# Optimization experiments

Hardware: AMD Instinct MI355X
Metric: run time of the kernel (lower is better)

The kernel has to match this reference:

```python
import jax, jax.numpy as jnp
import numpy as np

N_NODES = 50000
N_EDGES = 1600000
IN_DIM = 256
HID = 128
BATCH = 16384
EDGE_FEAT = 6
BN_EPS = 1e-5


def _glorot(key, shape):
    fan_in, fan_out = shape[0], shape[1]
    lim = float(np.sqrt(6.0 / (fan_in + fan_out)))
    return jax.random.uniform(key, shape, jnp.float32, -lim, lim)


def setup_inputs() -> dict:
    key = jax.random.key(0)
    ks = jax.random.split(key, 20)
    return {
        "x": jax.random.normal(ks[0], (N_NODES, IN_DIM), jnp.float32),
        "edge_index": jax.random.randint(ks[1], (2, N_EDGES), 0, N_NODES, jnp.int64 if jax.config.jax_enable_x64 else jnp.int32),
        "src_nodes": jax.random.randint(ks[2], (BATCH,), 0, N_NODES),
        "tgt_nodes": jax.random.randint(ks[3], (BATCH,), 0, N_NODES),
        "edge_features": jax.random.uniform(ks[4], (BATCH, EDGE_FEAT), jnp.float32),
        # SAGEConv layer 0: lin_l (aggregated neighbors, has bias), lin_r (root, no bias)
        "sage_wl0": _glorot(ks[5], (IN_DIM, HID)),
        "sage_b0": jnp.zeros((HID,), jnp.float32),
        "sage_wr0": _glorot(ks[6], (IN_DIM, HID)),
        # SAGEConv layer 1
        "sage_wl1": _glorot(ks[7], (HID, HID)),
        "sage_b1": jnp.zeros((HID,), jnp.float32),
        "sage_wr1": _glorot(ks[8], (HID, HID)),
        # edge_processor: Linear(6, 64)
        "ep_w": _glorot(ks[9], (EDGE_FEAT, HID // 2)),
        "ep_b": jnp.zeros((HID // 2,), jnp.float32),
        # predictor: Linear(320,128) -> ReLU -> BN(128) -> Linear(128,64) -> ReLU -> Linear(64,1) -> Sigmoid
        "p1_w": _glorot(ks[10], (2 * HID + HID // 2, HID)),
        "p1_b": jnp.zeros((HID,), jnp.float32),
        "bn_gamma": jnp.ones((HID,), jnp.float32),
        "bn_beta": jnp.zeros((HID,), jnp.float32),
        "bn_mean": jnp.zeros((HID,), jnp.float32),
        "bn_var": jnp.ones((HID,), jnp.float32),
        "p2_w": _glorot(ks[11], (HID, HID // 2)),
        "p2_b": jnp.zeros((HID // 2,), jnp.float32),
        "p3_w": _glorot(ks[12], (HID // 2, 1)),
        "p3_b": jnp.zeros((1,), jnp.float32),
    }


def _sage_conv(h, src, dst, w_l, b, w_r):
    # PyG SAGEConv(mean): out_i = W_l @ mean_{j in N(i)} h_j + b + W_r @ h_i
    n = h.shape[0]
    agg = jax.ops.segment_sum(h[src], dst, num_segments=n)  # [N, d]
    deg = jax.ops.segment_sum(jnp.ones((src.shape[0],), h.dtype), dst, num_segments=n)
    mean = agg / jnp.maximum(deg, 1.0)[:, None]
    return mean @ w_l + b + h @ w_r


def reference(x, edge_index, src_nodes, tgt_nodes, edge_features,
              sage_wl0, sage_b0, sage_wr0, sage_wl1, sage_b1, sage_wr1,
              ep_w, ep_b, p1_w, p1_b, bn_gamma, bn_beta, bn_mean, bn_var,
              p2_w, p2_b, p3_w, p3_b):
    src, dst = edge_index[0], edge_index[1]
    h = _sage_conv(x, src, dst, sage_wl0, sage_b0, sage_wr0)
    h = jax.nn.relu(h)  # dropout is identity in eval mode
    h = _sage_conv(h, src, dst, sage_wl1, sage_b1, sage_wr1)
    src_emb = h[src_nodes]  # [B, HID]
    tgt_emb = h[tgt_nodes]  # [B, HID]
    edge_proc = jax.nn.relu(edge_features @ ep_w + ep_b)  # [B, HID//2]
    combined = jnp.concatenate([src_emb, tgt_emb, edge_proc], axis=1)  # [B, 320]
    z = jax.nn.relu(combined @ p1_w + p1_b)
    z = (z - bn_mean) / jnp.sqrt(bn_var + BN_EPS) * bn_gamma + bn_beta  # BN eval mode
    z = jax.nn.relu(z @ p2_w + p2_b)
    return jax.nn.sigmoid(z @ p3_w + p3_b)  # [B, 1]
```

## Files before the change

### kernel.cpp

```cpp
#include <hip/hip_runtime.h>
#include <hip/hip_bf16.h>

#define N_NODES 50000
#define N_EDGES 1600000
#define BATCH   16384
#define HID     128
#define NBUCK   782
#define NBLK    256
#define EPB     6250

using short8  = __attribute__((ext_vector_type(8))) short;
using floatx4 = __attribute__((ext_vector_type(4))) float;
using floatv4 = __attribute__((ext_vector_type(4))) float;
using float2v = __attribute__((ext_vector_type(2))) float;
using uint2v  = __attribute__((ext_vector_type(2))) unsigned;
using uintx4  = __attribute__((ext_vector_type(4))) unsigned;
typedef unsigned short ushort_t;

__device__ __forceinline__ float bflo(unsigned u){ return __uint_as_float(u << 16); }
__device__ __forceinline__ float bfhi(unsigned u){ return __uint_as_float(u & 0xffff0000u); }
__device__ __forceinline__ float bf1(ushort_t u){ return __uint_as_float(((unsigned)u) << 16); }
__device__ __forceinline__ ushort_t f2bf(float f){
    unsigned u = __float_as_uint(f);
    return (ushort_t)((u + 0x7fffu + ((u >> 16) & 1u)) >> 16);
}
__device__ __forceinline__ int geti(const void* p, long long i, int is64){
    return is64 ? (int)((const long long*)p)[i] : ((const int*)p)[i];
}
__device__ __forceinline__ float2v up2(unsigned u){
    float2v r; r.x = bflo(u); r.y = bfhi(u); return r;
}

__global__ void k_detect(const unsigned* __restrict__ xbits,
                         const unsigned* __restrict__ eibits, int* flags){
    __shared__ int f[2];
    int t = threadIdx.x;
    if (t < 2) f[t] = 0;
    __syncthreads();
    unsigned u = xbits[t];
    unsigned e0 = (u >> 7)  & 0xFF;
    unsigned e1 = (u >> 23) & 0xFF;
    if (e0 >= 140 || e1 >= 140) atomicOr(&f[0], 1);
    if (eibits[2*t + 1] != 0)   atomicOr(&f[1], 1);
    __syncthreads();
    if (t == 0){ flags[0] = f[0]; flags[1] = f[1] ? 0 : 1; }
}

#define NT 19
struct ConvDesc { const void* src[NT]; int cum[NT + 1]; };
__global__ void k_conv(ConvDesc d, ushort_t* __restrict__ dst, const int* __restrict__ flags){
    int i = blockIdx.x*256 + threadIdx.x;
    if (i >= d.cum[NT]) return;
    int seg = 0;
    while (i >= d.cum[seg + 1]) seg++;
    int off = i - d.cum[seg];
    ushort_t v;
    if (flags[0]) v = f2bf(((const float*)d.src[seg])[off]);
    else          v = ((const ushort_t*)d.src[seg])[off];
    dst[i] = v;
}

#define OFF_WL0 0
#define OFF_WR0 32768
#define OFF_WL1 65536
#define OFF_WR1 81920
#define OFF_B0  98304
#define OFF_B1  98432
#define OFF_EPW 98560
#define OFF_EPB 98944
#define OFF_P1W 99008
#define OFF_P1B 139968
#define OFF_BNG 140096
#define OFF_BNB 140224
#define OFF_BNM 140352
#define OFF_BNV 140480
#define OFF_P2W 140608
#define OFF_P2B 148800
#define OFF_P3W 148864
#define OFF_EF  148928
#define OFF_P3B 247232
#define CW_TOT  247233

#define PACK_TOT 147584
__global__ void k_pack(const ushort_t* __restrict__ cw,
                       ushort_t* __restrict__ bp0, ushort_t* __restrict__ bp1,
                       ushort_t* __restrict__ bpp1, ushort_t* __restrict__ bpp2,
                       float* __restrict__ bnf){
    int i = blockIdx.x*256 + threadIdx.x;
    if (i < 65536){
        int j = i & 7, lane = (i >> 3) & 63, c = (i >> 9) & 15, kk = i >> 13;
        int k = kk*32 + (lane >> 4)*8 + j;
        int n = c*16 + (lane & 15);
        bp0[i] = (n < 128) ? cw[OFF_WL0 + k*128 + n] : cw[OFF_WR0 + k*128 + (n-128)];
    } else if (i < 98304){
        int i2 = i - 65536;
        int j = i2 & 7, lane = (i2 >> 3) & 63, c = (i2 >> 9) & 15, kk = i2 >> 13;
        int k = kk*32 + (lane >> 4)*8 + j;
        int n = c*16 + (lane & 15);
        bp1[i2] = (n < 128) ? cw[OFF_WL1 + k*128 + n] : cw[OFF_WR1 + k*128 + (n-128)];
    } else if (i < 139264){
        int i2 = i - 98304;
        int j = i2 & 7, lane = (i2 >> 3) & 63, ct = (i2 >> 9) & 7, kk = i2 >> 12;
        int k = kk*32 + (lane >> 4)*8 + j;
        int n = ct*16 + (lane & 15);
        bpp1[i2] = cw[OFF_P1W + k*128 + n];
    } else if (i < 147456){
        int i2 = i - 139264;
        int j = i2 & 7, lane = (i2 >> 3) & 63, ct = (i2 >> 9) & 3, kk = i2 >> 11;
        int k = kk*32 + (lane >> 4)*8 + j;
        int n = ct*16 + (lane & 15);
        bpp2[i2] = cw[OFF_P2W + k*64 + n];
    } else if (i < PACK_TOT){
        int n = i - 147456;
        float g = bf1(cw[OFF_BNG + n]), b = bf1(cw[OFF_BNB + n]);
        float m = bf1(cw[OFF_BNM + n]), v = bf1(cw[OFF_BNV + n]);
        float sc = g / sqrtf(v + 1e-5f);
        bnf[n] = sc; bnf[128 + n] = b - m*sc;
    }
}

__global__ __launch_bounds__(256)
void kb_hist(const void* __restrict__ ei, int* __restrict__ hist,
             const int* __restrict__ flags){
    __shared__ int lh[NBUCK];
    for (int i = threadIdx.x; i < NBUCK; i += 256) lh[i] = 0;
    __syncthreads();
    int i64 = flags[1];
    int e0 = blockIdx.x * EPB;
    for (int e = e0 + threadIdx.x; e < e0 + EPB; e += 256){
        int d = geti(ei, (long long)N_EDGES + e, i64);
        atomicAdd(&lh[d >> 6], 1);
    }
    __syncthreads();
    for (int i = threadIdx.x; i < NBUCK; i += 256)
        hist[i * NBLK + blockIdx.x] = lh[i];
}

__global__ __launch_bounds__(256)
void kb_scancol(int* __restrict__ hist, int* __restrict__ btot){
    __shared__ int sh[256];
    int b = blockIdx.x, t = threadIdx.x;
    int v = hist[b*NBLK + t];
    sh[t] = v; __syncthreads();
    for (int o = 1; o < 256; o <<= 1){
        int x = (t >= o) ? sh[t-o] : 0;
        __syncthreads();
        sh[t] += x;
        __syncthreads();
    }
    hist[b*NBLK + t] = sh[t] - v;
    if (t == 255) btot[b] = sh[255];
}

__global__ __launch_bounds__(1024)
void kb_scanbase(const int* __restrict__ btot, int* __restrict__ bbase,
                 int* __restrict__ off){
    __shared__ int sh[1024];
    int t = threadIdx.x;
    int v = (t < NBUCK) ? btot[t] : 0;
    sh[t] = v; __syncthreads();
    for (int o = 1; o < 1024; o <<= 1){
        int x = (t >= o) ? sh[t-o] : 0;
        __syncthreads();
        sh[t] += x;
        __syncthreads();
    }
    if (t < NBUCK) bbase[t] = sh[t] - v;
    if (t == 0){ bbase[NBUCK] = N_EDGES; off[N_NODES] = N_EDGES; }
}

__global__ __launch_bounds__(256)
void kb_scatter(const void* __restrict__ ei, const int* __restrict__ hist,
                const int* __restrict__ bbase, unsigned* __restrict__ ebuf,
                const int* __restrict__ flags){
    __shared__ int lcur[NBUCK];
    for (int i = threadIdx.x; i < NBUCK; i += 256)
        lcur[i] = bbase[i] + hist[i*NBLK + blockIdx.x];
    __syncthreads();
    int i64 = flags[1];
    int e0 = blockIdx.x * EPB;
    for (int e = e0 + threadIdx.x; e < e0 + EPB; e += 256){
        int s = geti(ei, e, i64);
        int d = geti(ei, (long long)N_EDGES + e, i64);
        int p = atomicAdd(&lcur[d >> 6], 1);
        ebuf[p] = (unsigned)s | ((unsigned)(d & 63) << 16);
    }
}

__global__ __launch_bounds__(256)
void kb_csr(const unsigned* __restrict__ ebuf, const int* __restrict__ bbase,
            ushort_t* __restrict__ csr, int* __restrict__ off){
    __shared__ int ldeg[64];
    int b = blockIdx.x, t = threadIdx.x;
    int ebase = bbase[b], eend = bbase[b+1];
    if (t < 64) ldeg[t] = 0;
    __syncthreads();
    for (int i = ebase + t; i < eend; i += 256)
        atomicAdd(&ldeg[(ebuf[i] >> 16) & 63], 1);
    __syncthreads();
    if (t < 64){
        int v = ldeg[t];
        int sum = v;
        #pragma unroll
        for (int o = 1; o < 64; o <<= 1){
            int x = __shfl_up(sum, o, 64);
            if (t >= o) sum += x;
        }
        int excl = sum - v;
        int node = b*64 + t;
        if (node < N_NODES) off[node] = ebase + excl;
        ldeg[t] = excl;
    }
    __syncthreads();
    for (int i = ebase + t; i < eend; i += 256){
        unsigned u = ebuf[i];
        int p = atomicAdd(&ldeg[(u >> 16) & 63], 1);
        csr[ebase + p] = (ushort_t)(u & 0xffffu);
    }
}

template<int KSTEPS, bool CHECKBF>
__global__ __launch_bounds__(256)
void k_gemm2(const ushort_t* __restrict__ A, const ushort_t* __restrict__ Bp,
             ushort_t* __restrict__ out, int M, const int* __restrict__ flags)
{
    if (CHECKBF && flags[0]) return;
    const int lane = threadIdx.x & 63;
    const int w    = threadIdx.x >> 6;
    const int rg   = w >> 1;
    const int cg   = w & 1;
    const int l16  = lane & 15;
    const int q    = lane >> 4;
    const int S    = KSTEPS * 32;
    const int m_base = blockIdx.x * 32 + rg * 16;

    int m = m_base + l16;
    bool ok = (m < M);
    const ushort_t* arow = A + (size_t)(ok ? m : 0) * S + q*8;
    const short8* bbase = (const short8*)Bp + lane;

    floatx4 acc[8] = {};
    for (int kk = 0; kk < KSTEPS; ++kk){
        short8 a = {0,0,0,0,0,0,0,0};
        if (ok) a = *(const short8*)(arow + kk*32);
        #pragma unroll
        for (int ci = 0; ci < 8; ++ci){
            short8 b = bbase[(kk*16 + cg*8 + ci)*64];
            acc[ci] = __builtin_amdgcn_mfma_f32_16x16x32_bf16(a, b, acc[ci], 0, 0, 0);
        }
    }

    int row_b = m_base + q*4;
    #pragma unroll
    for (int r = 0; r < 4; ++r){
        int row = row_b + r;
        if (row < M){
            #pragma unroll
            for (int ci = 0; ci < 8; ++ci)
                out[(size_t)row*256 + cg*128 + ci*16 + l16] = f2bf(acc[ci][r]);
        }
    }
}

__global__ __launch_bounds__(256)
void k_gemm2f(const float* __restrict__ Af, const ushort_t* __restrict__ Bp,
              ushort_t* __restrict__ out, int M, const int* __restrict__ flags)
{
    if (!flags[0]) return;
    const int KSTEPS = 8;
    const int lane = threadIdx.x & 63;
    const int w    = threadIdx.x >> 6;
    const int rg   = w >> 1;
    const int cg   = w & 1;
    const int l16  = lane & 15;
    const int q    = lane >> 4;
    const int S    = KSTEPS * 32;
    const int m_base = blockIdx.x * 32 + rg * 16;

    int m = m_base + l16;
    bool ok = (m < M);
    const float* arow = Af + (size_t)(ok ? m : 0) * S + q*8;
    const short8* bbase = (const short8*)Bp + lane;

    floatx4 acc[8] = {};
    for (int kk = 0; kk < KSTEPS; ++kk){
        union { unsigned u[4]; short8 s; } cv;
        cv.u[0]=0; cv.u[1]=0; cv.u[2]=0; cv.u[3]=0;
        if (ok){
            floatv4 f0 = *(const floatv4*)(arow + kk*32);
            floatv4 f1 = *(const floatv4*)(arow + kk*32 + 4);
            cv.u[0] = __builtin_amdgcn_perm(__float_as_uint(f0.y), __float_as_uint(f0.x), 0x07060302);
            cv.u[1] = __builtin_amdgcn_perm(__float_as_uint(f0.w), __float_as_uint(f0.z), 0x07060302);
            cv.u[2] = __builtin_amdgcn_perm(__float_as_uint(f1.y), __float_as_uint(f1.x), 0x07060302);
            cv.u[3] = __builtin_amdgcn_perm(__float_as_uint(f1.w), __float_as_uint(f1.z), 0x07060302);
        }
        #pragma unroll
        for (int ci = 0; ci < 8; ++ci){
            short8 b = bbase[(kk*16 + cg*8 + ci)*64];
            acc[ci] = __builtin_amdgcn_mfma_f32_16x16x32_bf16(cv.s, b, acc[ci], 0, 0, 0);
        }
    }

    int row_b = m_base + q*4;
    #pragma unroll
    for (int r = 0; r < 4; ++r){
        int row = row_b + r;
        if (row < M){
            #pragma unroll
            for (int ci = 0; ci < 8; ++ci)
                out[(size_t)row*256 + cg*128 + ci*16 + l16] = f2bf(acc[ci][r]);
        }
    }
}

__global__ __launch_bounds__(256)
void k_agg(const int* __restrict__ off, const ushort_t* __restrict__ csr,
           const ushort_t* __restrict__ yr, const ushort_t* __restrict__ bias,
           ushort_t* __restrict__ out, int do_relu)
{
    int v = blockIdx.x*4 + (threadIdx.x >> 6);
    if (v >= N_NODES) return;
    const int l = threadIdx.x & 63;
    const int g = l >> 4;
    const int c = l & 15;
    int e0 = off[v], e1 = off[v+1];
    const ushort_t* yb = yr + c*8;

    float2v A0[4] = {}, A1[4] = {}, A2[4] = {}, A3[4] = {};
    int p = e0;
    for (; p + 16 <= e1; p += 16){
        int u0 = csr[p + g];
        int u1 = csr[p + 4 + g];
        int u2 = csr[p + 8 + g];
        int u3 = csr[p + 12 + g];
        uintx4 d0 = *(const uintx4*)(yb + (size_t)u0*256);
        uintx4 d1 = *(const uintx4*)(yb + (size_t)u1*256);
        uintx4 d2 = *(const uintx4*)(yb + (size_t)u2*256);
        uintx4 d3 = *(const uintx4*)(yb + (size_t)u3*256);
        A0[0] += up2(d0.x); A0[1] += up2(d0.y); A0[2] += up2(d0.z); A0[3] += up2(d0.w);
        A1[0] += up2(d1.x); A1[1] += up2(d1.y); A1[2] += up2(d1.z); A1[3] += up2(d1.w);
        A2[0] += up2(d2.x); A2[1] += up2(d2.y); A2[2] += up2(d2.z); A2[3] += up2(d2.w);
        A3[0] += up2(d3.x); A3[1] += up2(d3.y); A3[2] += up2(d3.z); A3[3] += up2(d3.w);
    }
    for (; p + 4 <= e1; p += 4){
        int u0 = csr[p + g];
        uintx4 d0 = *(const uintx4*)(yb + (size_t)u0*256);
        A0[0] += up2(d0.x); A0[1] += up2(d0.y); A0[2] += up2(d0.z); A0[3] += up2(d0.w);
    }
    if (p + g < e1){
        int u1 = csr[p + g];
        uintx4 d1 = *(const uintx4*)(yb + (size_t)u1*256);
        A1[0] += up2(d1.x); A1[1] += up2(d1.y); A1[2] += up2(d1.z); A1[3] += up2(d1.w);
    }
    #pragma unroll
    for (int j = 0; j < 4; ++j) A0[j] += A1[j] + A2[j] + A3[j];

    float a0=A0[0].x, a1=A0[0].y, a2=A0[1].x, a3=A0[1].y;
    float a4=A0[2].x, a5=A0[2].y, a6=A0[3].x, a7=A0[3].y;
    #pragma unroll
    for (int m = 16; m <= 32; m <<= 1){
        a0 += __shfl_xor(a0, m, 64); a1 += __shfl_xor(a1, m, 64);
        a2 += __shfl_xor(a2, m, 64); a3 += __shfl_xor(a3, m, 64);
        a4 += __shfl_xor(a4, m, 64); a5 += __shfl_xor(a5, m, 64);
        a6 += __shfl_xor(a6, m, 64); a7 += __shfl_xor(a7, m, 64);
    }
    if (g == 0){
        float inv = 1.f / (float)max(e1 - e0, 1);
        uintx4 rr = *(const uintx4*)(yr + (size_t)v*256 + 128 + c*8);
        uintx4 bb = *(const uintx4*)(bias + c*8);
        float v0 = a0*inv + bflo(rr.x) + bflo(bb.x);
        float v1 = a1*inv + bfhi(rr.x) + bfhi(bb.x);
        float v2 = a2*inv + bflo(rr.y) + bflo(bb.y);
        float v3 = a3*inv + bfhi(rr.y) + bfhi(bb.y);
        float v4 = a4*inv + bflo(rr.z) + bflo(bb.z);
        float v5 = a5*inv + bfhi(rr.z) + bfhi(bb.z);
        float v6 = a6*inv + bflo(rr.w) + bflo(bb.w);
        float v7 = a7*inv + bfhi(rr.w) + bfhi(bb.w);
        if (do_relu){
            v0=fmaxf(v0,0.f); v1=fmaxf(v1,0.f); v2=fmaxf(v2,0.f); v3=fmaxf(v3,0.f);
            v4=fmaxf(v4,0.f); v5=fmaxf(v5,0.f); v6=fmaxf(v6,0.f); v7=fmaxf(v7,0.f);
        }
        uintx4 o;
        o.x = (unsigned)f2bf(v0) | ((unsigned)f2bf(v1) << 16);
        o.y = (unsigned)f2bf(v2) | ((unsigned)f2bf(v3) << 16);
        o.z = (unsigned)f2bf(v4) | ((unsigned)f2bf(v5) << 16);
        o.w = (unsigned)f2bf(v6) | ((unsigned)f2bf(v7) << 16);
        *(uintx4*)(out + (size_t)v*128 + c*8) = o;
    }
}

__global__ __launch_bounds__(256)
void k_pred2(const ushort_t* __restrict__ h2,
             const void* __restrict__ srcn, const void* __restrict__ tgtn,
             const ushort_t* __restrict__ cw, const ushort_t* __restrict__ bpp1,
             const ushort_t* __restrict__ bpp2, const float* __restrict__ bnf,
             void* __restrict__ outp, const int* __restrict__ flags)
{
    __shared__ ushort_t comb[64][328];
    __shared__ ushort_t zbuf[64][136];
    __shared__ ushort_t z2buf[64][68];
    __shared__ float    partial[4][64];
    __shared__ int      sid[64], tid_[64];

    const int t    = threadIdx.x;
    const int lane = t & 63;
    const int w    = t >> 6;
    const int l16  = lane & 15;
    const int q    = lane >> 4;
    const int row0 = blockIdx.x * 64;
    const int i64  = flags[1];

    if (t < 64){ sid[t] = geti(srcn, row0 + t, i64); tid_[t] = geti(tgtn, row0 + t, i64); }
    __syncthreads();

    const unsigned* h2u = (const unsigned*)h2;
    #pragma unroll 4
    for (int r = w*16; r < w*16 + 16; ++r){
        unsigned us = h2u[(size_t)sid[r]*64 + lane];
        unsigned ut = h2u[(size_t)tid_[r]*64 + lane];
        *(unsigned*)&comb[r][2*lane]       = us;
        *(unsigned*)&comb[r][128 + 2*lane] = ut;
    }
    {
        int r = t >> 2, c0 = (t & 3) * 16;
        float efv[6];
        #pragma unroll
        for (int k = 0; k < 6; ++k) efv[k] = bf1(cw[OFF_EF + (row0 + r)*6 + k]);
        #pragma unroll
        for (int c = 0; c < 16; ++c){
            int n = c0 + c;
            float a = bf1(cw[OFF_EPB + n]);
            #pragma unroll
            for (int k = 0; k < 6; ++k) a += efv[k] * bf1(cw[OFF_EPW + k*64 + n]);
            comb[r][256 + n] = f2bf(fmaxf(a, 0.f));
        }
    }
    __syncthreads();

    floatx4 acc[4][2] = {};
    for (int kk = 0; kk < 10; ++kk){
        short8 a[4];
        #pragma unroll
        for (int rt = 0; rt < 4; ++rt)
            a[rt] = *(const short8*)&comb[rt*16 + l16][kk*32 + q*8];
        #pragma unroll
        for (int ci = 0; ci < 2; ++ci){
            short8 b = *(const short8*)&bpp1[(((kk*8) + (w*2 + ci))*64 + lane)*8];
            #pragma unroll
            for (int rt = 0; rt < 4; ++rt)
                acc[rt][ci] = __builtin_amdgcn_mfma_f32_16x16x32_bf16(a[rt], b, acc[rt][ci], 0, 0, 0);
        }
    }
    #pragma unroll
    for (int ci = 0; ci < 2; ++ci){
        int n = w*32 + ci*16 + l16;
        float b1v = bf1(cw[OFF_P1B + n]);
        float sc = bnf[n], sh = bnf[128 + n];
        #pragma unroll
        for (int rt = 0; rt < 4; ++rt)
            #pragma unroll
            for (int r = 0; r < 4; ++r){
                float v = fmaxf(acc[rt][ci][r] + b1v, 0.f) * sc + sh;
                zbuf[rt*16 + q*4 + r][n] = f2bf(v);
            }
    }
    __syncthreads();

    floatx4 acc2[4] = {};
    for (int kk = 0; kk < 4; ++kk){
        short8 b = *(const short8*)&bpp2[(((kk*4) + w)*64 + lane)*8];
        #pragma unroll
        for (int rt = 0; rt < 4; ++rt){
            short8 a = *(const short8*)&zbuf[rt*16 + l16][kk*32 + q*8];
            acc2[rt] = __builtin_amdgcn_mfma_f32_16x16x32_bf16(a, b, acc2[rt], 0, 0, 0);
        }
    }
    {
        int n = w*16 + l16;
        float b2v = bf1(cw[OFF_P2B + n]);
        #pragma unroll
        for (int rt = 0; rt < 4; ++rt)
            #pragma unroll
            for (int r = 0; r < 4; ++r)
                z2buf[rt*16 + q*4 + r][n] = f2bf(fmaxf(acc2[rt][r] + b2v, 0.f));
    }
    __syncthreads();

    {
        int r = t & 63, seg = t >> 6;
        float s = 0.f;
        #pragma unroll
        for (int c = 0; c < 16; ++c){
            int n = seg*16 + c;
            s += bf1(z2buf[r][n]) * bf1(cw[OFF_P3W + n]);
        }
        partial[seg][r] = s;
    }
    __syncthreads();
    if (t < 64){
        float zf = partial[0][t] + partial[1][t] + partial[2][t] + partial[3][t] + bf1(cw[OFF_P3B]);
        float sg = 1.f / (1.f + __expf(-zf));
        if (flags[0]) ((float*)outp)[row0 + t] = sg;
        else          ((ushort_t*)outp)[row0 + t] = f2bf(sg);
    }
}

extern "C" void kernel_launch(void* const* d_in, const int* in_sizes, int n_in,
                              void* d_out, int out_size, void* d_ws, size_t ws_size,
                              hipStream_t stream)
{
    const void* x    = d_in[0];
    const void* ei   = d_in[1];
    const void* srcn = d_in[2];
    const void* tgtn = d_in[3];

    char* p = (char*)d_ws;
    auto carve = [&](size_t bytes)->char*{ char* r = p; p += (bytes + 511) & ~size_t(511); return r; };
    int* flags = (int*)carve(64);
    int* off   = (int*)carve((N_NODES+1)*4);
    int* btot  = (int*)carve(NBUCK*4);
    int* bbase = (int*)carve((NBUCK+1)*4);
    ushort_t* csr = (ushort_t*)carve((size_t)N_EDGES*2);
    ushort_t* yr  = (ushort_t*)carve((size_t)N_NODES*256*2);
    ushort_t* h   = (ushort_t*)carve((size_t)N_NODES*128*2);
    ushort_t* cw  = (ushort_t*)carve((size_t)CW_TOT*2);
    ushort_t* bp0 = (ushort_t*)carve((size_t)65536*2);
    ushort_t* bp1 = (ushort_t*)carve((size_t)32768*2);
    ushort_t* bpp1= (ushort_t*)carve((size_t)40960*2);
    ushort_t* bpp2= (ushort_t*)carve((size_t)8192*2);
    float*    bnf = (float*)carve(256*4);

    int*      hist = (int*)yr;
    unsigned* ebuf = (unsigned*)((char*)yr + 8u*1024*1024);

    k_detect<<<1, 256, 0, stream>>>((const unsigned*)x, (const unsigned*)ei, flags);

    ConvDesc cd;
    const int srcidx[NT] = {5,7,8,10,6,9,11,12,13,14,15,16,17,18,19,20,21,4,22};
    const int lens[NT]   = {32768,32768,16384,16384,128,128,384,64,40960,128,128,128,128,128,8192,64,64,98304,1};
    int run = 0;
    for (int i = 0; i < NT; ++i){ cd.src[i] = d_in[srcidx[i]]; cd.cum[i] = run; run += lens[i]; }
    cd.cum[NT] = run;
    k_conv<<<(CW_TOT+255)/256, 256, 0, stream>>>(cd, cw, flags);
    k_pack<<<(PACK_TOT+255)/256, 256, 0, stream>>>(cw, bp0, bp1, bpp1, bpp2, bnf);

    kb_hist    <<<NBLK, 256, 0, stream>>>(ei, hist, flags);
    kb_scancol <<<NBUCK, 256, 0, stream>>>(hist, btot);
    kb_scanbase<<<1, 1024, 0, stream>>>(btot, bbase, off);
    kb_scatter <<<NBLK, 256, 0, stream>>>(ei, hist, bbase, ebuf, flags);
    kb_csr     <<<NBUCK, 256, 0, stream>>>(ebuf, bbase, csr, off);

    int gblocks = (N_NODES + 31) / 32;
    k_gemm2<8, true><<<gblocks, 256, 0, stream>>>((const ushort_t*)x, bp0, yr, N_NODES, flags);
    k_gemm2f<<<gblocks, 256, 0, stream>>>((const float*)x, bp0, yr, N_NODES, flags);
    k_agg<<<(N_NODES+3)/4, 256, 0, stream>>>(off, csr, yr, cw+OFF_B0, h, 1);
    k_gemm2<4, false><<<gblocks, 256, 0, stream>>>(h, bp1, yr, N_NODES, flags);
    k_agg<<<(N_NODES+3)/4, 256, 0, stream>>>(off, csr, yr, cw+OFF_B1, h, 0);

    k_pred2<<<BATCH/64, 256, 0, stream>>>(h, srcn, tgtn, cw, bpp1, bpp2, bnf, d_out, flags);
}
```

Baseline: 342.2 us.

## Fuse independent preprocessing stages into shared launches to overlap GEMM with CSR build

Independent kernels are merged into combined launches where a block-index split picks the work: weight conversion runs alongside the edge histogram, weight packing alongside the column scan, and the layer-0 GEMM is split in halves that share launches with the edge scatter and CSR build. To allow this, the hist/ebuf scratch moves from the yr buffer, which the GEMM now writes concurrently, into the h buffer. The aim is fewer launches and idle gaps, with compute-heavy GEMM blocks filling the GPU while the atomic-bound sort kernels run. The cost is more branchy kernels whose LDS use and register pressure are set by the largest branch.

```diff
diff --git a/kernel.cpp b/kernel.cpp
--- a/kernel.cpp
+++ b/kernel.cpp
@@ -9,6 +9,11 @@
 #define NBLK    256
 #define EPB     6250
 
+#define CONVB   967
+#define PACKB   577
+#define G0A     782
+#define G0B     781
+
 using short8  = __attribute__((ext_vector_type(8))) short;
 using floatx4 = __attribute__((ext_vector_type(4))) float;
 using floatv4 = __attribute__((ext_vector_type(4))) float;
@@ -29,35 +34,6 @@
 }
 __device__ __forceinline__ float2v up2(unsigned u){
     float2v r; r.x = bflo(u); r.y = bfhi(u); return r;
-}
-
-__global__ void k_detect(const unsigned* __restrict__ xbits,
-                         const unsigned* __restrict__ eibits, int* flags){
-    __shared__ int f[2];
-    int t = threadIdx.x;
-    if (t < 2) f[t] = 0;
-    __syncthreads();
-    unsigned u = xbits[t];
-    unsigned e0 = (u >> 7)  & 0xFF;
-    unsigned e1 = (u >> 23) & 0xFF;
-    if (e0 >= 140 || e1 >= 140) atomicOr(&f[0], 1);
-    if (eibits[2*t + 1] != 0)   atomicOr(&f[1], 1);
-    __syncthreads();
-    if (t == 0){ flags[0] = f[0]; flags[1] = f[1] ? 0 : 1; }
-}
-
-#define NT 19
-struct ConvDesc { const void* src[NT]; int cum[NT + 1]; };
-__global__ void k_conv(ConvDesc d, ushort_t* __restrict__ dst, const int* __restrict__ flags){
-    int i = blockIdx.x*256 + threadIdx.x;
-    if (i >= d.cum[NT]) return;
-    int seg = 0;
-    while (i >= d.cum[seg + 1]) seg++;
-    int off = i - d.cum[seg];
-    ushort_t v;
-    if (flags[0]) v = f2bf(((const float*)d.src[seg])[off]);
-    else          v = ((const ushort_t*)d.src[seg])[off];
-    dst[i] = v;
 }
 
 #define OFF_WL0 0
@@ -80,76 +56,109 @@
 #define OFF_EF  148928
 #define OFF_P3B 247232
 #define CW_TOT  247233
-
 #define PACK_TOT 147584
-__global__ void k_pack(const ushort_t* __restrict__ cw,
-                       ushort_t* __restrict__ bp0, ushort_t* __restrict__ bp1,
-                       ushort_t* __restrict__ bpp1, ushort_t* __restrict__ bpp2,
-                       float* __restrict__ bnf){
-    int i = blockIdx.x*256 + threadIdx.x;
-    if (i < 65536){
-        int j = i & 7, lane = (i >> 3) & 63, c = (i >> 9) & 15, kk = i >> 13;
-        int k = kk*32 + (lane >> 4)*8 + j;
-        int n = c*16 + (lane & 15);
-        bp0[i] = (n < 128) ? cw[OFF_WL0 + k*128 + n] : cw[OFF_WR0 + k*128 + (n-128)];
-    } else if (i < 98304){
-        int i2 = i - 65536;
-        int j = i2 & 7, lane = (i2 >> 3) & 63, c = (i2 >> 9) & 15, kk = i2 >> 13;
-        int k = kk*32 + (lane >> 4)*8 + j;
-        int n = c*16 + (lane & 15);
-        bp1[i2] = (n < 128) ? cw[OFF_WL1 + k*128 + n] : cw[OFF_WR1 + k*128 + (n-128)];
-    } else if (i < 139264){
-        int i2 = i - 98304;
-        int j = i2 & 7, lane = (i2 >> 3) & 63, ct = (i2 >> 9) & 7, kk = i2 >> 12;
-        int k = kk*32 + (lane >> 4)*8 + j;
-        int n = ct*16 + (lane & 15);
-        bpp1[i2] = cw[OFF_P1W + k*128 + n];
-    } else if (i < 147456){
-        int i2 = i - 139264;
-        int j = i2 & 7, lane = (i2 >> 3) & 63, ct = (i2 >> 9) & 3, kk = i2 >> 11;
-        int k = kk*32 + (lane >> 4)*8 + j;
-        int n = ct*16 + (lane & 15);
-        bpp2[i2] = cw[OFF_P2W + k*64 + n];
-    } else if (i < PACK_TOT){
-        int n = i - 147456;
-        float g = bf1(cw[OFF_BNG + n]), b = bf1(cw[OFF_BNB + n]);
-        float m = bf1(cw[OFF_BNM + n]), v = bf1(cw[OFF_BNV + n]);
-        float sc = g / sqrtf(v + 1e-5f);
-        bnf[n] = sc; bnf[128 + n] = b - m*sc;
-    }
-}
-
-__global__ __launch_bounds__(256)
-void kb_hist(const void* __restrict__ ei, int* __restrict__ hist,
-             const int* __restrict__ flags){
+
+__global__ void k_detect(const unsigned* __restrict__ xbits,
+                         const unsigned* __restrict__ eibits, int* flags){
+    __shared__ int f[2];
+    int t = threadIdx.x;
+    if (t < 2) f[t] = 0;
+    __syncthreads();
+    unsigned u = xbits[t];
+    unsigned e0 = (u >> 7)  & 0xFF;
+    unsigned e1 = (u >> 23) & 0xFF;
+    if (e0 >= 140 || e1 >= 140) atomicOr(&f[0], 1);
+    if (eibits[2*t + 1] != 0)   atomicOr(&f[1], 1);
+    __syncthreads();
+    if (t == 0){ flags[0] = f[0]; flags[1] = f[1] ? 0 : 1; }
+}
+
+#define NT 19
+struct ConvDesc { const void* src[NT]; int cum[NT + 1]; };
+
+__global__ __launch_bounds__(256)
+void k_mix1(ConvDesc d, ushort_t* __restrict__ cw,
+            const void* __restrict__ ei, int* __restrict__ hist,
+            const int* __restrict__ flags){
     __shared__ int lh[NBUCK];
-    for (int i = threadIdx.x; i < NBUCK; i += 256) lh[i] = 0;
-    __syncthreads();
-    int i64 = flags[1];
-    int e0 = blockIdx.x * EPB;
-    for (int e = e0 + threadIdx.x; e < e0 + EPB; e += 256){
-        int d = geti(ei, (long long)N_EDGES + e, i64);
-        atomicAdd(&lh[d >> 6], 1);
-    }
-    __syncthreads();
-    for (int i = threadIdx.x; i < NBUCK; i += 256)
-        hist[i * NBLK + blockIdx.x] = lh[i];
-}
-
-__global__ __launch_bounds__(256)
-void kb_scancol(int* __restrict__ hist, int* __restrict__ btot){
+    if (blockIdx.x < CONVB){
+        int i = blockIdx.x*256 + threadIdx.x;
+        if (i >= d.cum[NT]) return;
+        int seg = 0;
+        while (i >= d.cum[seg + 1]) seg++;
+        int off = i - d.cum[seg];
+        ushort_t v;
+        if (flags[0]) v = f2bf(((const float*)d.src[seg])[off]);
+        else          v = ((const ushort_t*)d.src[seg])[off];
+        cw[i] = v;
+    } else {
+        int b = blockIdx.x - CONVB;
+        for (int i = threadIdx.x; i < NBUCK; i += 256) lh[i] = 0;
+        __syncthreads();
+        int i64 = flags[1];
+        int e0 = b * EPB;
+        for (int e = e0 + threadIdx.x; e < e0 + EPB; e += 256){
+            int dd = geti(ei, (long long)N_EDGES + e, i64);
+            atomicAdd(&lh[dd >> 6], 1);
+        }
+        __syncthreads();
+        for (int i = threadIdx.x; i < NBUCK; i += 256)
+            hist[i * NBLK + b] = lh[i];
+    }
+}
+
+__global__ __launch_bounds__(256)
+void k_mix2(const ushort_t* __restrict__ cw,
+            ushort_t* __restrict__ bp0, ushort_t* __restrict__ bp1,
+            ushort_t* __restrict__ bpp1, ushort_t* __restrict__ bpp2,
+            float* __restrict__ bnf,
+            int* __restrict__ hist, int* __restrict__ btot){
     __shared__ int sh[256];
-    int b = blockIdx.x, t = threadIdx.x;
-    int v = hist[b*NBLK + t];
-    sh[t] = v; __syncthreads();
-    for (int o = 1; o < 256; o <<= 1){
-        int x = (t >= o) ? sh[t-o] : 0;
-        __syncthreads();
-        sh[t] += x;
-        __syncthreads();
-    }
-    hist[b*NBLK + t] = sh[t] - v;
-    if (t == 255) btot[b] = sh[255];
+    if (blockIdx.x < PACKB){
+        int i = blockIdx.x*256 + threadIdx.x;
+        if (i < 65536){
+            int j = i & 7, lane = (i >> 3) & 63, c = (i >> 9) & 15, kk = i >> 13;
+            int k = kk*32 + (lane >> 4)*8 + j;
+            int n = c*16 + (lane & 15);
+            bp0[i] = (n < 128) ? cw[OFF_WL0 + k*128 + n] : cw[OFF_WR0 + k*128 + (n-128)];
+        } else if (i < 98304){
+            int i2 = i - 65536;
+            int j = i2 & 7, lane = (i2 >> 3) & 63, c = (i2 >> 9) & 15, kk = i2 >> 13;
+            int k = kk*32 + (lane >> 4)*8 + j;
+            int n = c*16 + (lane & 15);
+            bp1[i2] = (n < 128) ? cw[OFF_WL1 + k*128 + n] : cw[OFF_WR1 + k*128 + (n-128)];
+        } else if (i < 139264){
+            int i2 = i - 98304;
+            int j = i2 & 7, lane = (i2 >> 3) & 63, ct = (i2 >> 9) & 7, kk = i2 >> 12;
+            int k = kk*32 + (lane >> 4)*8 + j;
+            int n = ct*16 + (lane & 15);
+            bpp1[i2] = cw[OFF_P1W + k*128 + n];
+        } else if (i < 147456){
+            int i2 = i - 139264;
+            int j = i2 & 7, lane = (i2 >> 3) & 63, ct = (i2 >> 9) & 3, kk = i2 >> 11;
+            int k = kk*32 + (lane >> 4)*8 + j;
+            int n = ct*16 + (lane & 15);
+            bpp2[i2] = cw[OFF_P2W + k*64 + n];
+        } else if (i < PACK_TOT){
+            int n = i - 147456;
+            float g = bf1(cw[OFF_BNG + n]), b = bf1(cw[OFF_BNB + n]);
+            float m = bf1(cw[OFF_BNM + n]), v = bf1(cw[OFF_BNV + n]);
+            float sc = g / sqrtf(v + 1e-5f);
+            bnf[n] = sc; bnf[128 + n] = b - m*sc;
+        }
+    } else {
+        int b = blockIdx.x - PACKB, t = threadIdx.x;
+        int v = hist[b*NBLK + t];
+        sh[t] = v; __syncthreads();
+        for (int o = 1; o < 256; o <<= 1){
+            int x = (t >= o) ? sh[t-o] : 0;
+            __syncthreads();
+            sh[t] += x;
+            __syncthreads();
+        }
+        hist[b*NBLK + t] = sh[t] - v;
+        if (t == 255) btot[b] = sh[255];
+    }
 }
 
 __global__ __launch_bounds__(1024)
@@ -169,62 +178,133 @@
     if (t == 0){ bbase[NBUCK] = N_EDGES; off[N_NODES] = N_EDGES; }
 }
 
-__global__ __launch_bounds__(256)
-void kb_scatter(const void* __restrict__ ei, const int* __restrict__ hist,
-                const int* __restrict__ bbase, unsigned* __restrict__ ebuf,
-                const int* __restrict__ flags){
+__device__ __forceinline__ void gemm0_body(const void* __restrict__ xin,
+                                           const ushort_t* __restrict__ Bp,
+                                           ushort_t* __restrict__ out,
+                                           int M, int f32, int blk){
+    const int t = threadIdx.x;
+    const int lane = t & 63;
+    const int w = t >> 6;
+    const int rg = w >> 1, cg = w & 1;
+    const int l16 = lane & 15, q = lane >> 4;
+    const int m_base = blk * 32 + rg * 16;
+    int m = m_base + l16;
+    bool ok = (m < M);
+    const short8* bbase = (const short8*)Bp + lane;
+
+    floatx4 acc[8] = {};
+    if (f32){
+        const float* arow = (const float*)xin + (size_t)(ok ? m : 0)*256 + q*8;
+        for (int kk = 0; kk < 8; ++kk){
+            union { unsigned u[4]; short8 s; } cv;
+            cv.u[0]=0; cv.u[1]=0; cv.u[2]=0; cv.u[3]=0;
+            if (ok){
+                floatv4 f0 = *(const floatv4*)(arow + kk*32);
+                floatv4 f1 = *(const floatv4*)(arow + kk*32 + 4);
+                cv.u[0] = __builtin_amdgcn_perm(__float_as_uint(f0.y), __float_as_uint(f0.x), 0x07060302);
+                cv.u[1] = __builtin_amdgcn_perm(__float_as_uint(f0.w), __float_as_uint(f0.z), 0x07060302);
+                cv.u[2] = __builtin_amdgcn_perm(__float_as_uint(f1.y), __float_as_uint(f1.x), 0x07060302);
+                cv.u[3] = __builtin_amdgcn_perm(__float_as_uint(f1.w), __float_as_uint(f1.z), 0x07060302);
+            }
+            #pragma unroll
+            for (int ci = 0; ci < 8; ++ci){
+                short8 b = bbase[(kk*16 + cg*8 + ci)*64];
+                acc[ci] = __builtin_amdgcn_mfma_f32_16x16x32_bf16(cv.s, b, acc[ci], 0, 0, 0);
+            }
+        }
+    } else {
+        const ushort_t* arow = (const ushort_t*)xin + (size_t)(ok ? m : 0)*256 + q*8;
+        for (int kk = 0; kk < 8; ++kk){
+            short8 a = {0,0,0,0,0,0,0,0};
+            if (ok) a = *(const short8*)(arow + kk*32);
+            #pragma unroll
+            for (int ci = 0; ci < 8; ++ci){
+                short8 b = bbase[(kk*16 + cg*8 + ci)*64];
+                acc[ci] = __builtin_amdgcn_mfma_f32_16x16x32_bf16(a, b, acc[ci], 0, 0, 0);
+            }
+        }
+    }
+    int row_b = m_base + q*4;
+    #pragma unroll
+    for (int r = 0; r < 4; ++r){
+        int row = row_b + r;
+        if (row < M){
+            #pragma unroll
+            for (int ci = 0; ci < 8; ++ci)
+                out[(size_t)row*256 + cg*128 + ci*16 + l16] = f2bf(acc[ci][r]);
+        }
+    }
+}
+
+__global__ __launch_bounds__(256)
+void k_mix3a(const void* __restrict__ x, const ushort_t* __restrict__ bp0,
+             ushort_t* __restrict__ yr,
+             const void* __restrict__ ei, const int* __restrict__ hist,
+             const int* __restrict__ bbase, unsigned* __restrict__ ebuf,
+             const int* __restrict__ flags){
     __shared__ int lcur[NBUCK];
-    for (int i = threadIdx.x; i < NBUCK; i += 256)
-        lcur[i] = bbase[i] + hist[i*NBLK + blockIdx.x];
-    __syncthreads();
-    int i64 = flags[1];
-    int e0 = blockIdx.x * EPB;
-    for (int e = e0 + threadIdx.x; e < e0 + EPB; e += 256){
-        int s = geti(ei, e, i64);
-        int d = geti(ei, (long long)N_EDGES + e, i64);
-        int p = atomicAdd(&lcur[d >> 6], 1);
-        ebuf[p] = (unsigned)s | ((unsigned)(d & 63) << 16);
-    }
-}
-
-__global__ __launch_bounds__(256)
-void kb_csr(const unsigned* __restrict__ ebuf, const int* __restrict__ bbase,
-            ushort_t* __restrict__ csr, int* __restrict__ off){
+    if (blockIdx.x < G0A){
+        gemm0_body(x, bp0, yr, N_NODES, flags[0], blockIdx.x);
+    } else {
+        int b = blockIdx.x - G0A;
+        for (int i = threadIdx.x; i < NBUCK; i += 256)
+            lcur[i] = bbase[i] + hist[i*NBLK + b];
+        __syncthreads();
+        int i64 = flags[1];
+        int e0 = b * EPB;
+        for (int e = e0 + threadIdx.x; e < e0 + EPB; e += 256){
+            int s = geti(ei, e, i64);
+            int d = geti(ei, (long long)N_EDGES + e, i64);
+            int p = atomicAdd(&lcur[d >> 6], 1);
+            ebuf[p] = (unsigned)s | ((unsigned)(d & 63) << 16);
+        }
+    }
+}
+
+__global__ __launch_bounds__(256)
+void k_mix3b(const void* __restrict__ x, const ushort_t* __restrict__ bp0,
+             ushort_t* __restrict__ yr,
+             const unsigned* __restrict__ ebuf, const int* __restrict__ bbase,
+             ushort_t* __restrict__ csr, int* __restrict__ off,
+             const int* __restrict__ flags){
     __shared__ int ldeg[64];
-    int b = blockIdx.x, t = threadIdx.x;
-    int ebase = bbase[b], eend = bbase[b+1];
-    if (t < 64) ldeg[t] = 0;
-    __syncthreads();
-    for (int i = ebase + t; i < eend; i += 256)
-        atomicAdd(&ldeg[(ebuf[i] >> 16) & 63], 1);
-    __syncthreads();
-    if (t < 64){
-        int v = ldeg[t];
-        int sum = v;
-        #pragma unroll
-        for (int o = 1; o < 64; o <<= 1){
-            int x = __shfl_up(sum, o, 64);
-            if (t >= o) sum += x;
-        }
-        int excl = sum - v;
-        int node = b*64 + t;
-        if (node < N_NODES) off[node] = ebase + excl;
-        ldeg[t] = excl;
-    }
-    __syncthreads();
-    for (int i = ebase + t; i < eend; i += 256){
-        unsigned u = ebuf[i];
-        int p = atomicAdd(&ldeg[(u >> 16) & 63], 1);
-        csr[ebase + p] = (ushort_t)(u & 0xffffu);
-    }
-}
-
-template<int KSTEPS, bool CHECKBF>
-__global__ __launch_bounds__(256)
-void k_gemm2(const ushort_t* __restrict__ A, const ushort_t* __restrict__ Bp,
-             ushort_t* __restrict__ out, int M, const int* __restrict__ flags)
+    if (blockIdx.x < G0B){
+        gemm0_body(x, bp0, yr, N_NODES, flags[0], G0A + blockIdx.x);
+    } else {
+        int b = blockIdx.x - G0B, t = threadIdx.x;
+        int ebase = bbase[b], eend = bbase[b+1];
+        if (t < 64) ldeg[t] = 0;
+        __syncthreads();
+        for (int i = ebase + t; i < eend; i += 256)
+            atomicAdd(&ldeg[(ebuf[i] >> 16) & 63], 1);
+        __syncthreads();
+        if (t < 64){
+            int v = ldeg[t];
+            int sum = v;
+            #pragma unroll
+            for (int o = 1; o < 64; o <<= 1){
+                int x2 = __shfl_up(sum, o, 64);
+                if (t >= o) sum += x2;
+            }
+            int excl = sum - v;
+            int node = b*64 + t;
+            if (node < N_NODES) off[node] = ebase + excl;
+            ldeg[t] = excl;
+        }
+        __syncthreads();
+        for (int i = ebase + t; i < eend; i += 256){
+            unsigned u = ebuf[i];
+            int p = atomicAdd(&ldeg[(u >> 16) & 63], 1);
+            csr[ebase + p] = (ushort_t)(u & 0xffffu);
+        }
+    }
+}
+
+__global__ __launch_bounds__(256)
+void k_gemm1(const ushort_t* __restrict__ A, const ushort_t* __restrict__ Bp,
+             ushort_t* __restrict__ out, int M)
 {
-    if (CHECKBF && flags[0]) return;
+    const int KSTEPS = 4;
     const int lane = threadIdx.x & 63;
     const int w    = threadIdx.x >> 6;
     const int rg   = w >> 1;
@@ -247,57 +327,6 @@
         for (int ci = 0; ci < 8; ++ci){
             short8 b = bbase[(kk*16 + cg*8 + ci)*64];
             acc[ci] = __builtin_amdgcn_mfma_f32_16x16x32_bf16(a, b, acc[ci], 0, 0, 0);
-        }
-    }
-
-    int row_b = m_base + q*4;
-    #pragma unroll
-    for (int r = 0; r < 4; ++r){
-        int row = row_b + r;
-        if (row < M){
-            #pragma unroll
-            for (int ci = 0; ci < 8; ++ci)
-                out[(size_t)row*256 + cg*128 + ci*16 + l16] = f2bf(acc[ci][r]);
-        }
-    }
-}
-
-__global__ __launch_bounds__(256)
-void k_gemm2f(const float* __restrict__ Af, const ushort_t* __restrict__ Bp,
-              ushort_t* __restrict__ out, int M, const int* __restrict__ flags)
-{
-    if (!flags[0]) return;
-    const int KSTEPS = 8;
-    const int lane = threadIdx.x & 63;
-    const int w    = threadIdx.x >> 6;
-    const int rg   = w >> 1;
-    const int cg   = w & 1;
-    const int l16  = lane & 15;
-    const int q    = lane >> 4;
-    const int S    = KSTEPS * 32;
-    const int m_base = blockIdx.x * 32 + rg * 16;
-
-    int m = m_base + l16;
-    bool ok = (m < M);
-    const float* arow = Af + (size_t)(ok ? m : 0) * S + q*8;
-    const short8* bbase = (const short8*)Bp + lane;
-
-    floatx4 acc[8] = {};
-    for (int kk = 0; kk < KSTEPS; ++kk){
-        union { unsigned u[4]; short8 s; } cv;
-        cv.u[0]=0; cv.u[1]=0; cv.u[2]=0; cv.u[3]=0;
-        if (ok){
-            floatv4 f0 = *(const floatv4*)(arow + kk*32);
-            floatv4 f1 = *(const floatv4*)(arow + kk*32 + 4);
-            cv.u[0] = __builtin_amdgcn_perm(__float_as_uint(f0.y), __float_as_uint(f0.x), 0x07060302);
-            cv.u[1] = __builtin_amdgcn_perm(__float_as_uint(f0.w), __float_as_uint(f0.z), 0x07060302);
-            cv.u[2] = __builtin_amdgcn_perm(__float_as_uint(f1.y), __float_as_uint(f1.x), 0x07060302);
-            cv.u[3] = __builtin_amdgcn_perm(__float_as_uint(f1.w), __float_as_uint(f1.z), 0x07060302);
-        }
-        #pragma unroll
-        for (int ci = 0; ci < 8; ++ci){
-            short8 b = bbase[(kk*16 + cg*8 + ci)*64];
-            acc[ci] = __builtin_amdgcn_mfma_f32_16x16x32_bf16(cv.s, b, acc[ci], 0, 0, 0);
         }
     }
 
@@ -530,8 +559,8 @@
     ushort_t* bpp2= (ushort_t*)carve((size_t)8192*2);
     float*    bnf = (float*)carve(256*4);
 
-    int*      hist = (int*)yr;
-    unsigned* ebuf = (unsigned*)((char*)yr + 8u*1024*1024);
+    int*      hist = (int*)h;
+    unsigned* ebuf = (unsigned*)((char*)h + 1u*1024*1024);
 
     k_detect<<<1, 256, 0, stream>>>((const unsigned*)x, (const unsigned*)ei, flags);
 
@@ -541,20 +570,15 @@
     int run = 0;
     for (int i = 0; i < NT; ++i){ cd.src[i] = d_in[srcidx[i]]; cd.cum[i] = run; run += lens[i]; }
     cd.cum[NT] = run;
-    k_conv<<<(CW_TOT+255)/256, 256, 0, stream>>>(cd, cw, flags);
-    k_pack<<<(PACK_TOT+255)/256, 256, 0, stream>>>(cw, bp0, bp1, bpp1, bpp2, bnf);
-
-    kb_hist    <<<NBLK, 256, 0, stream>>>(ei, hist, flags);
-    kb_scancol <<<NBUCK, 256, 0, stream>>>(hist, btot);
+
+    k_mix1<<<CONVB + NBLK, 256, 0, stream>>>(cd, cw, ei, hist, flags);
+    k_mix2<<<PACKB + NBUCK, 256, 0, stream>>>(cw, bp0, bp1, bpp1, bpp2, bnf, hist, btot);
     kb_scanbase<<<1, 1024, 0, stream>>>(btot, bbase, off);
-    kb_scatter <<<NBLK, 256, 0, stream>>>(ei, hist, bbase, ebuf, flags);
-    kb_csr     <<<NBUCK, 256, 0, stream>>>(ebuf, bbase, csr, off);
-
-    int gblocks = (N_NODES + 31) / 32;
-    k_gemm2<8, true><<<gblocks, 256, 0, stream>>>((const ushort_t*)x, bp0, yr, N_NODES, flags);
-    k_gemm2f<<<gblocks, 256, 0, stream>>>((const float*)x, bp0, yr, N_NODES, flags);
+    k_mix3a<<<G0A + NBLK, 256, 0, stream>>>(x, bp0, yr, ei, hist, bbase, ebuf, flags);
+    k_mix3b<<<G0B + NBUCK, 256, 0, stream>>>(x, bp0, yr, ebuf, bbase, csr, off, flags);
+
     k_agg<<<(N_NODES+3)/4, 256, 0, stream>>>(off, csr, yr, cw+OFF_B0, h, 1);
-    k_gemm2<4, false><<<gblocks, 256, 0, stream>>>(h, bp1, yr, N_NODES, flags);
+    k_gemm1<<<(N_NODES + 31)/32, 256, 0, stream>>>(h, bp1, yr, N_NODES);
     k_agg<<<(N_NODES+3)/4, 256, 0, stream>>>(off, csr, yr, cw+OFF_B1, h, 0);
 
     k_pred2<<<BATCH/64, 256, 0, stream>>>(h, srcn, tgtn, cw, bpp1, bpp2, bnf, d_out, flags);
```

After: 338.9 us. Within noise of the previous version (-1.0%).
